# Kernel optimization log

Measured on AMD Instinct MI355X. Metric: run time of the kernel, lower is better.

## Reference

```python
import jax, jax.numpy as jnp
import numpy as np

D_MODEL = 2048
NUM_HEADS = 16
D_HEAD = D_MODEL // NUM_HEADS


def setup_inputs() -> dict:
    key = jax.random.key(0)
    k_x, k_q, k_k, k_v, k_o, k_ob = jax.random.split(key, 6)
    B, L = 2, 2048
    s = 1.0 / np.sqrt(D_MODEL)
    return {
        "x": jax.random.normal(k_x, (B, L, D_MODEL), dtype=jnp.float32),
        # torch nn.Linear weights are (out_features, in_features)
        "Wq": jax.random.uniform(k_q, (D_MODEL, D_MODEL), jnp.float32, -s, s),
        "Wk": jax.random.uniform(k_k, (D_HEAD, D_MODEL), jnp.float32, -s, s),
        "Wv": jax.random.uniform(k_v, (D_HEAD, D_MODEL), jnp.float32, -s, s),
        "Wo": jax.random.uniform(k_o, (D_MODEL, D_MODEL), jnp.float32, -s, s),
        "bo": jax.random.uniform(k_ob, (D_MODEL,), jnp.float32, -s, s),
    }


def reference(x, Wq, Wk, Wv, Wo, bo):
    B, L, _ = x.shape
    H, dh = NUM_HEADS, D_HEAD
    Q = (x @ Wq.T).reshape(B, L, H, dh).transpose(0, 2, 1, 3)  # [B,H,L,dh]
    K = x @ Wk.T  # [B,L,dh] shared across heads (MQA)
    V = x @ Wv.T  # [B,L,dh]
    scores = jnp.einsum("bhqd,bkd->bhqk", Q, K) / np.sqrt(dh)  # [B,H,L,L]
    attn = jax.nn.softmax(scores, axis=-1)
    out = jnp.einsum("bhqk,bkd->bhqd", attn, V)  # [B,H,L,dh]
    out = out.transpose(0, 2, 1, 3).reshape(B, L, H * dh)
    return out @ Wo.T + bo
```

## Files before the change

kernel.cpp:

```cpp
#include <hip/hip_runtime.h>


typedef __attribute__((ext_vector_type(8))) short bf16x8;
typedef __attribute__((ext_vector_type(4))) short short4v;
typedef __attribute__((ext_vector_type(4))) float f32x4;
typedef __attribute__((ext_vector_type(16))) float f32x16;
typedef __attribute__((ext_vector_type(4))) int int4v;

__device__ __forceinline__ unsigned short f2bf(float f) {
  unsigned int u = __builtin_bit_cast(unsigned int, f);
  u += 0x7fffu + ((u >> 16) & 1u);
  return (unsigned short)(u >> 16);
}

__device__ __forceinline__ unsigned int cvtpk(float lo, float hi) {
  unsigned int r;
  asm("v_cvt_pk_bf16_f32 %0, %1, %2" : "=v"(r) : "v"(lo), "v"(hi));
  return r;
}

typedef __attribute__((address_space(1))) void gvoid_t;
typedef __attribute__((address_space(3))) void lvoid_t;

__device__ __forceinline__ void gll16(const void* g, void* l) {
  __builtin_amdgcn_global_load_lds((gvoid_t*)g, (lvoid_t*)l, 16, 0, 0);
}

__global__ void cast_all_kernel(
    const float* __restrict__ x, const float* __restrict__ wq,
    const float* __restrict__ wk, const float* __restrict__ wv,
    const float* __restrict__ wo, unsigned short* __restrict__ xb,
    unsigned short* __restrict__ wallb, unsigned short* __restrict__ wob) {
  const int NT = 4325376;
  int i = blockIdx.x * blockDim.x + threadIdx.x;
  const int stride = gridDim.x * blockDim.x;
  for (; i < NT; i += stride) {
    const float* src;
    unsigned short* dst;
    int j;
    if (i < 2097152) {
      src = x; dst = xb; j = i;
    } else if (i < 3145728) {
      src = wq; dst = wallb; j = i - 2097152;
    } else if (i < 3211264) {
      src = wk; dst = wallb + 2048 * 2048; j = i - 3145728;
    } else if (i < 3276800) {
      src = wv; dst = wallb + 2176 * 2048; j = i - 3211264;
    } else {
      src = wo; dst = wob; j = i - 3276800;
    }
    float4 f = reinterpret_cast<const float4*>(src)[j];
    short4v o;
    o.x = (short)f2bf(f.x);
    o.y = (short)f2bf(f.y);
    o.z = (short)f2bf(f.z);
    o.w = (short)f2bf(f.w);
    reinterpret_cast<short4v*>(dst)[j] = o;
  }
}

template <int MODE>
__global__ __launch_bounds__(256) void gemm_bt(
    const unsigned short* __restrict__ A, const unsigned short* __restrict__ B,
    void* __restrict__ Cout, int M, int N, int K, float scale,
    const float* __restrict__ bias, void* __restrict__ C2,
    void* __restrict__ C3) {
  __shared__ unsigned short As[128 * 64] __attribute__((aligned(16)));
  __shared__ unsigned short Bs[128 * 64] __attribute__((aligned(16)));

  const int tid = threadIdx.x;
  const int lane = tid & 63;
  const int wave = tid >> 6;
  const int lr = lane & 15;
  const int lg = lane >> 4;
  const int bm = blockIdx.x * 128;
  const int bn = blockIdx.y * 128;
  const int wrow = (wave >> 1) * 64;
  const int wcol = (wave & 1) * 64;

  f32x4 acc[4][4] = {};

  int soff[4];
#pragma unroll
  for (int t = 0; t < 4; t++) {
    int ci = t * 256 + tid;
    int row = ci >> 3;
    int c = (ci ^ row) & 7;
    soff[t] = row * K + c * 8;
  }
  const unsigned short* Abase = A + (size_t)bm * K;
  const unsigned short* Bbase = B + (size_t)bn * K;

  for (int k0 = 0; k0 < K; k0 += 64) {
    __syncthreads();
#pragma unroll
    for (int t = 0; t < 4; t++) {
      gll16(Abase + k0 + soff[t], (char*)As + (t * 256 + tid) * 16);
      gll16(Bbase + k0 + soff[t], (char*)Bs + (t * 256 + tid) * 16);
    }
    __syncthreads();

#pragma unroll
    for (int kh = 0; kh < 2; kh++) {
      bf16x8 af[4], bfr[4];
#pragma unroll
      for (int mi = 0; mi < 4; mi++) {
        const int row = wrow + mi * 16 + lr;
        const int ch = (lg + 4 * kh) ^ (row & 7);
        af[mi] = *(const bf16x8*)&As[row * 64 + ch * 8];
      }
#pragma unroll
      for (int nj = 0; nj < 4; nj++) {
        const int row = wcol + nj * 16 + lr;
        const int ch = (lg + 4 * kh) ^ (row & 7);
        bfr[nj] = *(const bf16x8*)&Bs[row * 64 + ch * 8];
      }
#pragma unroll
      for (int mi = 0; mi < 4; mi++)
#pragma unroll
        for (int nj = 0; nj < 4; nj++)
          acc[mi][nj] = __builtin_amdgcn_mfma_f32_16x16x32_bf16(
              af[mi], bfr[nj], acc[mi][nj], 0, 0, 0);
    }
  }

#pragma unroll
  for (int mi = 0; mi < 4; mi++)
#pragma unroll
    for (int nj = 0; nj < 4; nj++) {
      const int row = bm + wrow + mi * 16 + (lane >> 4) * 4;
      const int col = bn + wcol + nj * 16 + lr;
#pragma unroll
      for (int r = 0; r < 4; r++) {
        float v = acc[mi][nj][r];
        if constexpr (MODE == 2) {
          ((float*)Cout)[(size_t)(row + r) * N + col] = v + bias[col];
        } else {
          if (col < 2048)
            ((unsigned short*)Cout)[(size_t)(row + r) * 2048 + col] =
                f2bf(v * scale);
          else if (col < 2176)
            ((unsigned short*)C2)[(size_t)(row + r) * 128 + (col - 2048)] =
                f2bf(v);
          else
            ((unsigned short*)C3)[(size_t)(col - 2176) * M + (row + r)] =
                f2bf(v);
        }
      }
    }
}

__global__ __launch_bounds__(256, 3) void mqa_attn(
    const unsigned short* __restrict__ Q, const unsigned short* __restrict__ Kb,
    const unsigned short* __restrict__ VT, unsigned short* __restrict__ Ob) {
  __shared__ unsigned short Ksm[2][8192] __attribute__((aligned(16)));
  __shared__ unsigned short Vsm[8192] __attribute__((aligned(16)));

  const int tid = threadIdx.x;
  const int lane = tid & 63;
  const int wi = tid >> 6;
  const int l31 = lane & 31;
  const int hi = lane >> 5;
  const int bh = blockIdx.y;
  const int b = bh >> 4;
  const int h = bh & 15;
  const int q0 = blockIdx.x * 128 + wi * 32;

  const unsigned short* Qb = Q + ((size_t)(b * 2048 + q0)) * 2048 + h * 128;
  const unsigned short* Kbase = Kb + (size_t)b * 2048 * 128;
  const unsigned short* VTb = VT + (size_t)b * 2048;

  bf16x8 qf[8];
#pragma unroll
  for (int ks = 0; ks < 8; ks++)
    qf[ks] = *(const bf16x8*)&Qb[(size_t)l31 * 2048 + ks * 16 + hi * 8];

  f32x16 oacc[4] = {};
  float lrun = 0.0f;

  int koff[4], voff[4];
#pragma unroll
  for (int t = 0; t < 4; t++) {
    int ci = t * 256 + tid;
    int row = ci >> 4;
    int p = (ci ^ row) & 15;
    koff[t] = row * 128 + p * 8;
    voff[t] = (2 * row + (p >> 3)) * 4096 + (p & 7) * 8;
  }

  auto stageK = [&](int kv0, int bsel) {
    const unsigned short* kp = Kbase + (size_t)kv0 * 128;
    char* kb = (char*)&Ksm[bsel][0];
#pragma unroll
    for (int t = 0; t < 4; t++) gll16(kp + koff[t], kb + (t * 256 + tid) * 16);
  };
  auto stageV = [&](int kv0) {
    const unsigned short* vp = VTb + kv0;
    char* vb = (char*)&Vsm[0];
#pragma unroll
    for (int t = 0; t < 4; t++) gll16(vp + voff[t], vb + (t * 256 + tid) * 16);
  };

  stageK(0, 0);
  stageV(0);
  asm volatile("s_waitcnt vmcnt(0)" ::: "memory");
  __builtin_amdgcn_sched_barrier(0);
  __builtin_amdgcn_s_barrier();

  for (int t = 0; t < 32; t++) {
    const int cur = t & 1;
    stageK(((t + 1) & 31) * 64, cur ^ 1);
    const unsigned short* Kt = &Ksm[cur][0];
    const unsigned short* Vt = &Vsm[0];

    f32x16 st[2] = {};
#pragma unroll
    for (int ks = 0; ks < 8; ks++) {
#pragma unroll
      for (int sub = 0; sub < 2; sub++) {
        const int krow = sub * 32 + l31;
        const int pos = (2 * ks + hi) ^ (krow & 15);
        bf16x8 kf = *(const bf16x8*)&Kt[krow * 128 + pos * 8];
        st[sub] =
            __builtin_amdgcn_mfma_f32_32x32x16_bf16(kf, qf[ks], st[sub], 0, 0, 0);
      }
    }

#pragma unroll
    for (int sub = 0; sub < 2; sub++)
#pragma unroll
      for (int r = 0; r < 16; r++)
        st[sub][r] = __builtin_amdgcn_exp2f(st[sub][r]);
    {
      float s0 = (st[0][0] + st[0][1]) + (st[0][2] + st[0][3]);
      float s1 = (st[0][4] + st[0][5]) + (st[0][6] + st[0][7]);
      float s2 = (st[0][8] + st[0][9]) + (st[0][10] + st[0][11]);
      float s3 = (st[0][12] + st[0][13]) + (st[0][14] + st[0][15]);
      float s4 = (st[1][0] + st[1][1]) + (st[1][2] + st[1][3]);
      float s5 = (st[1][4] + st[1][5]) + (st[1][6] + st[1][7]);
      float s6 = (st[1][8] + st[1][9]) + (st[1][10] + st[1][11]);
      float s7 = (st[1][12] + st[1][13]) + (st[1][14] + st[1][15]);
      float ps = ((s0 + s1) + (s2 + s3)) + ((s4 + s5) + (s6 + s7));
      lrun += ps + __shfl_xor(ps, 32);
    }

    bf16x8 paw[4];
#pragma unroll
    for (int sub = 0; sub < 2; sub++)
#pragma unroll
      for (int h2 = 0; h2 < 2; h2++) {
        unsigned int a0 = cvtpk(st[sub][8 * h2 + 0], st[sub][8 * h2 + 1]);
        unsigned int a1 = cvtpk(st[sub][8 * h2 + 2], st[sub][8 * h2 + 3]);
        unsigned int b0 = cvtpk(st[sub][8 * h2 + 4], st[sub][8 * h2 + 5]);
        unsigned int b1 = cvtpk(st[sub][8 * h2 + 6], st[sub][8 * h2 + 7]);
        unsigned int s0 = hi ? a0 : b0;
        unsigned int s1 = hi ? a1 : b1;
        unsigned int r0 = (unsigned int)__shfl_xor((int)s0, 32);
        unsigned int r1 = (unsigned int)__shfl_xor((int)s1, 32);
        int4v w;
        w.x = (int)(hi ? r0 : a0);
        w.y = (int)(hi ? r1 : a1);
        w.z = (int)(hi ? b0 : r0);
        w.w = (int)(hi ? b1 : r1);
        paw[sub * 2 + h2] = __builtin_bit_cast(bf16x8, w);
      }

    asm volatile("s_waitcnt vmcnt(4)" ::: "memory");
    __builtin_amdgcn_sched_barrier(0);
    __builtin_amdgcn_s_barrier();

#pragma unroll
    for (int dt = 0; dt < 4; dt++) {
      f32x16 z = oacc[dt];
      const int s = dt * 16 + (l31 >> 1);
#pragma unroll
      for (int ks2 = 0; ks2 < 4; ks2++) {
        const int pos = (8 * (l31 & 1) + 2 * ks2 + hi) ^ (s & 15);
        bf16x8 vfr = *(const bf16x8*)&Vt[s * 128 + pos * 8];
        z = __builtin_amdgcn_mfma_f32_32x32x16_bf16(paw[ks2], vfr, z, 0, 0, 0);
      }
      oacc[dt] = z;
    }

    __builtin_amdgcn_s_barrier();
    stageV(((t + 1) & 31) * 64);
    asm volatile("s_waitcnt vmcnt(4)" ::: "memory");
    __builtin_amdgcn_sched_barrier(0);
    __builtin_amdgcn_s_barrier();
  }

  float linv = 1.0f / lrun;
#pragma unroll
  for (int r = 0; r < 16; r++) {
    const int qrow = (r & 3) + 8 * (r >> 2) + 4 * hi;
    float invr = __shfl(linv, qrow);
    size_t row = (size_t)(b * 2048 + q0 + qrow);
#pragma unroll
    for (int dt = 0; dt < 4; dt++)
      Ob[row * 2048 + h * 128 + dt * 32 + l31] = f2bf(oacc[dt][r] * invr);
  }
}

extern "C" void kernel_launch(void* const* d_in, const int* in_sizes, int n_in,
                              void* d_out, int out_size, void* d_ws,
                              size_t ws_size, hipStream_t stream) {
  const float* x = (const float*)d_in[0];
  const float* Wq = (const float*)d_in[1];
  const float* Wk = (const float*)d_in[2];
  const float* Wv = (const float*)d_in[3];
  const float* Wo = (const float*)d_in[4];
  const float* bo = (const float*)d_in[5];

  const int Bb = 2, Lq = 2048, D = 2048, DH = 128;
  const int M = Bb * Lq;

  char* ws = (char*)d_ws;
  size_t off = 0;
  auto alloc = [&](size_t bytes) {
    void* p = ws + off;
    off += (bytes + 255) & ~size_t(255);
    return p;
  };
  unsigned short* x_bf = (unsigned short*)alloc((size_t)M * D * 2);
  unsigned short* Wall_bf = (unsigned short*)alloc((size_t)2304 * D * 2);
  unsigned short* Wo_bf = (unsigned short*)alloc((size_t)D * D * 2);
  unsigned short* Qbuf = (unsigned short*)alloc((size_t)M * D * 2);
  unsigned short* Kbuf = (unsigned short*)alloc((size_t)M * DH * 2);
  unsigned short* VTbuf = (unsigned short*)alloc((size_t)DH * M * 2);
  unsigned short* AObuf = (unsigned short*)alloc((size_t)M * D * 2);

  cast_all_kernel<<<2048, 256, 0, stream>>>(x, Wq, Wk, Wv, Wo, x_bf, Wall_bf,
                                            Wo_bf);

  gemm_bt<4><<<dim3(M / 128, 2304 / 128), 256, 0, stream>>>(
      x_bf, Wall_bf, Qbuf, M, 2304, D, 0.12752041986f, nullptr, Kbuf, VTbuf);
  mqa_attn<<<dim3(Lq / 128, Bb * 16), 256, 0, stream>>>(Qbuf, Kbuf, VTbuf,
                                                        AObuf);
  gemm_bt<2><<<dim3(M / 128, D / 128), 256, 0, stream>>>(
      AObuf, Wo_bf, d_out, M, D, D, 1.0f, bo, nullptr, nullptr);
}
```

Baseline: 198.3 us.

## Load V fragments directly from global memory into registers, dropping V LDS staging

```diff
diff --git a/kernel.cpp b/kernel.cpp
--- a/kernel.cpp
+++ b/kernel.cpp
@@ -154,7 +154,6 @@
     const unsigned short* __restrict__ Q, const unsigned short* __restrict__ Kb,
     const unsigned short* __restrict__ VT, unsigned short* __restrict__ Ob) {
   __shared__ unsigned short Ksm[2][8192] __attribute__((aligned(16)));
-  __shared__ unsigned short Vsm[8192] __attribute__((aligned(16)));
 
   const int tid = threadIdx.x;
   const int lane = tid & 63;
@@ -175,17 +174,21 @@
   for (int ks = 0; ks < 8; ks++)
     qf[ks] = *(const bf16x8*)&Qb[(size_t)l31 * 2048 + ks * 16 + hi * 8];
 
+  const unsigned short* vrow[4];
+#pragma unroll
+  for (int dt = 0; dt < 4; dt++)
+    vrow[dt] = VTb + (size_t)(dt * 32 + l31) * 4096 + hi * 8;
+
   f32x16 oacc[4] = {};
   float lrun = 0.0f;
 
-  int koff[4], voff[4];
+  int koff[4];
 #pragma unroll
   for (int t = 0; t < 4; t++) {
     int ci = t * 256 + tid;
     int row = ci >> 4;
     int p = (ci ^ row) & 15;
     koff[t] = row * 128 + p * 8;
-    voff[t] = (2 * row + (p >> 3)) * 4096 + (p & 7) * 8;
   }
 
   auto stageK = [&](int kv0, int bsel) {
@@ -194,24 +197,27 @@
 #pragma unroll
     for (int t = 0; t < 4; t++) gll16(kp + koff[t], kb + (t * 256 + tid) * 16);
   };
-  auto stageV = [&](int kv0) {
-    const unsigned short* vp = VTb + kv0;
-    char* vb = (char*)&Vsm[0];
-#pragma unroll
-    for (int t = 0; t < 4; t++) gll16(vp + voff[t], vb + (t * 256 + tid) * 16);
-  };
 
   stageK(0, 0);
-  stageV(0);
   asm volatile("s_waitcnt vmcnt(0)" ::: "memory");
   __builtin_amdgcn_sched_barrier(0);
   __builtin_amdgcn_s_barrier();
 
   for (int t = 0; t < 32; t++) {
     const int cur = t & 1;
+    const int kv0 = t * 64;
+
+    bf16x8 vf[4][4];
+#pragma unroll
+    for (int dt = 0; dt < 4; dt++) {
+      const unsigned short* vr = vrow[dt] + kv0;
+#pragma unroll
+      for (int ks2 = 0; ks2 < 4; ks2++)
+        vf[dt][ks2] = *(const bf16x8*)(vr + ks2 * 16);
+    }
+
     stageK(((t + 1) & 31) * 64, cur ^ 1);
     const unsigned short* Kt = &Ksm[cur][0];
-    const unsigned short* Vt = &Vsm[0];
 
     f32x16 st[2] = {};
 #pragma unroll
@@ -221,8 +227,8 @@
         const int krow = sub * 32 + l31;
         const int pos = (2 * ks + hi) ^ (krow & 15);
         bf16x8 kf = *(const bf16x8*)&Kt[krow * 128 + pos * 8];
-        st[sub] =
-            __builtin_amdgcn_mfma_f32_32x32x16_bf16(kf, qf[ks], st[sub], 0, 0, 0);
+        st[sub] = __builtin_amdgcn_mfma_f32_32x32x16_bf16(kf, qf[ks], st[sub],
+                                                          0, 0, 0);
       }
     }
 
@@ -265,26 +271,17 @@
         paw[sub * 2 + h2] = __builtin_bit_cast(bf16x8, w);
       }
 
-    asm volatile("s_waitcnt vmcnt(4)" ::: "memory");
-    __builtin_amdgcn_sched_barrier(0);
-    __builtin_amdgcn_s_barrier();
-
 #pragma unroll
     for (int dt = 0; dt < 4; dt++) {
       f32x16 z = oacc[dt];
-      const int s = dt * 16 + (l31 >> 1);
-#pragma unroll
-      for (int ks2 = 0; ks2 < 4; ks2++) {
-        const int pos = (8 * (l31 & 1) + 2 * ks2 + hi) ^ (s & 15);
-        bf16x8 vfr = *(const bf16x8*)&Vt[s * 128 + pos * 8];
-        z = __builtin_amdgcn_mfma_f32_32x32x16_bf16(paw[ks2], vfr, z, 0, 0, 0);
-      }
+#pragma unroll
+      for (int ks2 = 0; ks2 < 4; ks2++)
+        z = __builtin_amdgcn_mfma_f32_32x32x16_bf16(paw[ks2], vf[dt][ks2], z,
+                                                    0, 0, 0);
       oacc[dt] = z;
     }
 
-    __builtin_amdgcn_s_barrier();
-    stageV(((t + 1) & 31) * 64);
-    asm volatile("s_waitcnt vmcnt(4)" ::: "memory");
+    asm volatile("s_waitcnt vmcnt(0)" ::: "memory");
     __builtin_amdgcn_sched_barrier(0);
     __builtin_amdgcn_s_barrier();
   }
```

Measured after the change: 284.9 us. +43.7%, slower.
